# Kernel tuning notes

Measured on AMD Instinct MI355X. Metric: run time of the kernel, lower is better.

## Reference

```python
import jax, jax.numpy as jnp
import numpy as np

POOL = (32, 32, 32)
P_ENC_DIM = 48
NON_LOCAL_ITER = 2


def _neighbor_graph(spatial):
    # connectivity=2 binary structure in 3x3x3 (k_size=3): 19 offsets with |dx|+|dy|+|dz| <= 2
    D, H, W = spatial
    offs = np.array([(dx, dy, dz) for dx in (-1, 0, 1) for dy in (-1, 0, 1) for dz in (-1, 0, 1)
                     if abs(dx) + abs(dy) + abs(dz) <= 2], dtype=np.int64)  # [K=19,3]
    coords = np.stack(np.meshgrid(np.arange(D), np.arange(H), np.arange(W), indexing='ij'), -1).reshape(-1, 3)
    nbr = coords[:, None, :] + offs[None]                                  # [N,K,3]
    valid = ((nbr >= 0) & (nbr < np.array([D, H, W]))).all(-1)             # [N,K] side nodes lose oob edges
    nbrc = np.clip(nbr, 0, np.array([D - 1, H - 1, W - 1]))
    idx = np.ravel_multi_index(nbrc.reshape(-1, 3).T, (D, H, W)).reshape(valid.shape)
    return jnp.asarray(idx, jnp.int32), jnp.asarray(valid)


def _build_pe(spatial, p_enc_dim, dtype=jnp.float32):
    # sin/cos positional encoding over 3D grid, interleaved per axis (build_geo_feature)
    D, H, W = spatial
    d_model = p_enc_dim // 3
    div = (1e-4) ** (jnp.arange(0, d_model, 2, dtype=dtype) / d_model)     # [d_model//2]
    grids = jnp.meshgrid(jnp.arange(D), jnp.arange(H), jnp.arange(W), indexing='ij')
    parts = []
    for d in range(3):
        ang = grids[d].astype(dtype)[None] * div[:, None, None, None]      # [h,D,H,W]
        parts.append(jnp.stack([jnp.sin(ang), jnp.cos(ang)], 1).reshape(d_model, D, H, W))
    pe = jnp.concatenate(parts, 0)                                         # [p_enc_dim,D,H,W]
    return pe.reshape(p_enc_dim, -1).T                                     # [N,p_enc_dim]


def setup_inputs():
    key = jax.random.key(0)
    ks = jax.random.split(key, 6)
    B, Cf, Cc, FD, GD = 2, 256, 21, 64, 64
    D, H, W = POOL
    neighbor_idx, nbr_mask = _neighbor_graph(POOL)

    def lin(k, fi, fo):
        return jax.random.normal(k, (fi, fo), jnp.float32) / np.sqrt(fi).astype(np.float32)

    return {
        'cam': jax.random.uniform(ks[0], (B, Cc, D, H, W), jnp.float32),
        'f': jax.random.normal(ks[1], (B, Cf, D, H, W), jnp.float32),
        'theta_w': lin(ks[2], Cf, FD), 'theta_b': jnp.zeros((FD,), jnp.float32),
        'phi_w': lin(ks[3], Cf, FD), 'phi_b': jnp.zeros((FD,), jnp.float32),
        'geo_theta_w': lin(ks[4], P_ENC_DIM, GD), 'geo_theta_b': jnp.zeros((GD,), jnp.float32),
        'geo_phi_w': lin(ks[5], P_ENC_DIM, GD), 'geo_phi_b': jnp.zeros((GD,), jnp.float32),
        'neighbor_idx': neighbor_idx, 'nbr_mask': nbr_mask,
    }


def reference(cam, f, theta_w, theta_b, phi_w, phi_b, geo_theta_w, geo_theta_b,
              geo_phi_w, geo_phi_b, neighbor_idx, nbr_mask):
    B, Cc, D, H, W = cam.shape
    N = D * H * W
    f_flat = f.reshape(B, f.shape[1], N).transpose(0, 2, 1)                # [B,N,Cf]
    x_theta = f_flat @ theta_w + theta_b                                    # [B,N,fd]
    x_phi = (f_flat @ phi_w + phi_b)[:, neighbor_idx]                       # [B,N,K,fd] gather
    pe = jax.lax.stop_gradient(_build_pe((D, H, W), P_ENC_DIM, cam.dtype))  # geo feature is detached
    g_theta = pe @ geo_theta_w + geo_theta_b                                # [N,gd]
    g_phi = (pe @ geo_phi_w + geo_phi_b)[neighbor_idx]                      # [N,K,gd]
    # merge_type 'scaled_dot_product_geo': f = theta.phi + geo_theta.geo_phi; softmax(f / sqrt(K))
    scores = jnp.einsum('bnd,bnkd->bnk', x_theta, x_phi) \
           + jnp.einsum('nd,nkd->nk', g_theta, g_phi)[None]
    Kn = scores.shape[-1]
    scores = scores / jnp.sqrt(jnp.asarray(Kn, scores.dtype))
    scores = jnp.where(nbr_mask[None], scores, -jnp.inf)                    # side nodes: fewer edges
    w = jax.nn.softmax(scores, axis=-1)                                     # [B,N,K]
    cam_flat = cam.reshape(B, Cc, N).transpose(0, 2, 1)                     # [B,N,Cc]
    for _ in range(NON_LOCAL_ITER):                                         # weights fixed (f unchanged)
        cam_flat = jnp.einsum('bnk,bnkc->bnc', w, cam_flat[:, neighbor_idx])
    return cam_flat.transpose(0, 2, 1).reshape(B, Cc, D, H, W)
```

## Files before the change

kernel.cpp:

```cpp
#include <hip/hip_runtime.h>
#include <hip/hip_bf16.h>
#include <hip/hip_fp16.h>

#define DD 32
#define HH 32
#define WW 32
#define NN 32768
#define BB 2
#define CF 256
#define CC 21
#define FD 64
#define KK 19

typedef __attribute__((ext_vector_type(8))) short bf16x8;
typedef __attribute__((ext_vector_type(4))) float f32x4;

__device__ const int OFF[19][3] = {
    {-1,-1, 0}, {-1, 0,-1}, {-1, 0, 0}, {-1, 0, 1}, {-1, 1, 0},
    { 0,-1,-1}, { 0,-1, 0}, { 0,-1, 1}, { 0, 0,-1}, { 0, 0, 0},
    { 0, 0, 1}, { 0, 1,-1}, { 0, 1, 0}, { 0, 1, 1},
    { 1,-1, 0}, { 1, 0,-1}, { 1, 0, 0}, { 1, 0, 1}, { 1, 1, 0}
};

__device__ __forceinline__ unsigned short f2bf(float x) {
    unsigned u = __float_as_uint(x);
    u += 0x7FFFu + ((u >> 16) & 1u);
    return (unsigned short)(u >> 16);
}

__global__ __launch_bounds__(256) void tbl_kernel(
    const float* __restrict__ gtw, const float* __restrict__ gtb,
    const float* __restrict__ gpw, const float* __restrict__ gpb,
    const float* __restrict__ thw, const float* __restrict__ phw,
    float* __restrict__ Tg, uint4* __restrict__ whi)
{
    int blk = blockIdx.x, tid = threadIdx.x;
    if (blk >= 10) {
        int gid = (blk - 10) * 256 + tid;
        int col = gid & 127;
        int g8 = gid >> 7;
        const float* src = (col < 64) ? (thw + col) : (phw + (col - 64));
        int kbase = g8 * 8;
        unsigned hi4[4];
#pragma unroll
        for (int e2 = 0; e2 < 4; ++e2) {
            float va = src[(kbase + 2 * e2) * 64];
            float vb = src[(kbase + 2 * e2 + 1) * 64];
            hi4[e2] = (unsigned)f2bf(va) | ((unsigned)f2bf(vb) << 16);
        }
        whi[g8 * 128 + col] = make_uint4(hi4[0], hi4[1], hi4[2], hi4[3]);
        return;
    }

    __shared__ float pe_s[32][16];
    for (int i = tid; i < 512; i += 256) {
        int c = i >> 4, q = i & 15;
        int ii = q >> 1;
        float div = expf(-9.210340371976184f * (float)ii * 0.125f);
        float ang = (float)c * div;
        pe_s[c][q] = (q & 1) ? cosf(ang) : sinf(ang);
    }
    __syncthreads();

    __shared__ float panels[6][32][65];
    int npan = (blk == 9) ? 6 : 2;
#pragma unroll 1
    for (int pp = 0; pp < npan; ++pp) {
        int axis, isP;
        if (blk == 9) { axis = pp % 3; isP = pp / 3; }
        else          { axis = (pp == 0) ? (blk / 3) : (blk % 3); isP = pp; }
        const float* W = isP ? gpw : gtw;
#pragma unroll
        for (int e = 0; e < 8; ++e) {
            int idx = e * 256 + tid;
            int c = idx >> 6, j = idx & 63;
            float acc = 0.f;
#pragma unroll
            for (int q = 0; q < 16; ++q)
                acc = fmaf(pe_s[c][q], W[(axis * 16 + q) * 64 + j], acc);
            panels[pp][c][j] = acc;
        }
    }
    __syncthreads();

    if (blk < 9) {
        bool tr = (blk == 6) || (blk == 7);
#pragma unroll
        for (int e = 0; e < 4; ++e) {
            int idx = e * 256 + tid;
            int x = idx >> 5, y = idx & 31;
            float s = 0.f;
#pragma unroll
            for (int j = 0; j < 64; ++j)
                s = fmaf(panels[0][x][j], panels[1][y][j], s);
            Tg[blk * 1024 + (tr ? (y * 32 + x) : (x * 32 + y))] = s;
        }
    } else {
        if (tid < 96) {
            int ax = tid >> 5, c = tid & 31;
            float s = 0.f;
#pragma unroll
            for (int j = 0; j < 64; ++j) s = fmaf(panels[ax][c][j], gpb[j], s);
            Tg[9216 + ax * 32 + c] = s;
        } else if (tid < 192) {
            int t2 = tid - 96;
            int ax = t2 >> 5, c = t2 & 31;
            float s = 0.f;
#pragma unroll
            for (int j = 0; j < 64; ++j) s = fmaf(gtb[j], panels[3 + ax][c][j], s);
            Tg[9312 + ax * 32 + c] = s;
        } else if (tid == 192) {
            float s = 0.f;
#pragma unroll
            for (int j = 0; j < 64; ++j) s = fmaf(gtb[j], gpb[j], s);
            Tg[9408] = s;
        }
    }
}

__global__ __launch_bounds__(256) void proj_kernel(
    const float* __restrict__ f, const uint4* __restrict__ whi,
    const float* __restrict__ thb, const float* __restrict__ phb,
    __half* __restrict__ theta, __half* __restrict__ phi)
{
    __shared__ __align__(16) unsigned short Ahi[128][8][8];
    __shared__ __align__(16) unsigned short Bhi[128][8][8];

    int tid = threadIdx.x;
    int b = blockIdx.x >> 8;
    int n0 = (blockIdx.x & 255) * 128;
    int wv = tid >> 6, lane = tid & 63;
    int wr = (wv >> 1) * 64, wc = (wv & 1) * 64;
    int fr = lane & 15, kb_r = lane >> 4;

    int srow = tid & 127;
    int kb0 = (tid >> 7) * 4;

    const float* fb = f + (size_t)b * CF * NN + n0;

    f32x4 acc[4][4];
#pragma unroll
    for (int mi = 0; mi < 4; ++mi)
#pragma unroll
        for (int ni = 0; ni < 4; ++ni) acc[mi][ni] = (f32x4){0.f, 0.f, 0.f, 0.f};

#pragma unroll 1
    for (int k0 = 0; k0 < CF; k0 += 64) {
#pragma unroll
        for (int i = 0; i < 4; ++i) {
            int kb = kb0 + i;
            const float* src = fb + (size_t)(k0 + kb * 8) * NN + srow;
            unsigned hi4[4];
#pragma unroll
            for (int e2 = 0; e2 < 4; ++e2) {
                float va = src[(size_t)(2 * e2) * NN];
                float vb = src[(size_t)(2 * e2 + 1) * NN];
                hi4[e2] = (unsigned)f2bf(va) | ((unsigned)f2bf(vb) << 16);
            }
            int slot = kb ^ (srow & 7);
            *(uint4*)&Ahi[srow][slot][0] = make_uint4(hi4[0], hi4[1], hi4[2], hi4[3]);
        }
        {
            const uint4* wh = whi + (size_t)(k0 >> 3) * 128;
#pragma unroll
            for (int i = 0; i < 4; ++i) {
                int kb = kb0 + i;
                uint4 hh = wh[kb * 128 + srow];
                int slot = kb ^ (srow & 7);
                *(uint4*)&Bhi[srow][slot][0] = hh;
            }
        }
        __syncthreads();
#pragma unroll
        for (int c = 0; c < 2; ++c) {
            bf16x8 ah[4], bh[4];
            int kb_c = c * 4 + kb_r;
#pragma unroll
            for (int mi = 0; mi < 4; ++mi) {
                int r = wr + mi * 16 + fr;
                int slot = kb_c ^ (r & 7);
                ah[mi] = *(const bf16x8*)&Ahi[r][slot][0];
            }
#pragma unroll
            for (int ni = 0; ni < 4; ++ni) {
                int col = wc + ni * 16 + fr;
                int slot = kb_c ^ (col & 7);
                bh[ni] = *(const bf16x8*)&Bhi[col][slot][0];
            }
#pragma unroll
            for (int mi = 0; mi < 4; ++mi)
#pragma unroll
                for (int ni = 0; ni < 4; ++ni)
                    acc[mi][ni] = __builtin_amdgcn_mfma_f32_16x16x32_bf16(ah[mi], bh[ni], acc[mi][ni], 0, 0, 0);
        }
        __syncthreads();
    }

#pragma unroll
    for (int ni = 0; ni < 4; ++ni) {
        int j = wc + ni * 16 + fr;
        float bj = (j < 64) ? thb[j] : phb[j - 64];
        __half* outp = (j < 64) ? (theta + (size_t)b * NN * 64 + j)
                                : (phi + (size_t)b * NN * 64 + (j - 64));
#pragma unroll
        for (int mi = 0; mi < 4; ++mi) {
            int nbase = n0 + wr + mi * 16 + kb_r * 4;
#pragma unroll
            for (int r = 0; r < 4; ++r)
                outp[(size_t)(nbase + r) * 64] = __float2half(acc[mi][ni][r] + bj);
        }
    }
}

__global__ __launch_bounds__(256) void gsc_kernel(
    const float* __restrict__ Tg, float* __restrict__ gsc)
{
    __shared__ float Ts[9 * 1024];
    __shared__ float UVs[193];
    int tid = threadIdx.x;
#pragma unroll
    for (int i = 0; i < 9; ++i) {
        int idx = i * 1024 + tid;
        Ts[idx] = Tg[idx];
        Ts[idx + 256] = Tg[idx + 256];
        Ts[idx + 512] = Tg[idx + 512];
        Ts[idx + 768] = Tg[idx + 768];
    }
    if (tid < 193) UVs[tid] = Tg[9216 + tid];
    __syncthreads();

    int n = blockIdx.x * 256 + tid;
    int d = n >> 10, h = (n >> 5) & 31, w = n & 31;
    float Un = UVs[d] + UVs[32 + h] + UVs[64 + w] + UVs[192];
    const float rs = 0.2294157338705618f;

#pragma unroll
    for (int k = 0; k < KK; ++k) {
        int nd = d + OFF[k][0], nh = h + OFF[k][1], nw = w + OFF[k][2];
        bool valid = ((unsigned)nd < 32u) && ((unsigned)nh < 32u) && ((unsigned)nw < 32u);
        int ndc = min(max(nd, 0), 31), nhc = min(max(nh, 0), 31), nwc = min(max(nw, 0), 31);
        float g = Ts[0 * 1024 + d * 32 + ndc] + Ts[1 * 1024 + d * 32 + nhc]
                + Ts[2 * 1024 + d * 32 + nwc] + Ts[3 * 1024 + h * 32 + ndc]
                + Ts[4 * 1024 + h * 32 + nhc] + Ts[5 * 1024 + h * 32 + nwc]
                + Ts[6 * 1024 + ndc * 32 + w] + Ts[7 * 1024 + nhc * 32 + w]
                + Ts[8 * 1024 + w * 32 + nwc]
                + Un + UVs[96 + ndc] + UVs[128 + nhc] + UVs[160 + nwc];
        gsc[(size_t)k * NN + n] = valid ? g * rs : -INFINITY;
    }
}

__global__ __launch_bounds__(256) void score_kernel(
    const __half* __restrict__ theta, const __half* __restrict__ phi,
    const float* __restrict__ gsc, float* __restrict__ wgt)
{
    int tid = threadIdx.x;
    int lane = tid & 63;
    int wv = tid >> 6;
    int sub = lane >> 4;
    int col4 = lane & 15;
    int gn = blockIdx.x * 16 + wv * 4 + sub;
    int b = gn >> 15;
    int n = gn & (NN - 1);
    int d = n >> 10, h = (n >> 5) & 31, w = n & 31;

    uint2 traw = *(const uint2*)(theta + (size_t)gn * 64 + col4 * 4);
    __half2 t01 = __builtin_bit_cast(__half2, traw.x);
    __half2 t23 = __builtin_bit_cast(__half2, traw.y);
    float2 tf01 = __half22float2(t01), tf23 = __half22float2(t23);
    float4 tq = {tf01.x, tf01.y, tf23.x, tf23.y};

    const __half* pb = phi + (size_t)b * NN * 64;
    const float* gr = gsc + n;
    const float rs = 0.2294157338705618f;

    float s[KK];
#pragma unroll
    for (int k = 0; k < KK; ++k) {
        int nd = d + OFF[k][0], nh = h + OFF[k][1], nw = w + OFF[k][2];
        nd = min(max(nd, 0), 31); nh = min(max(nh, 0), 31); nw = min(max(nw, 0), 31);
        int nn = (nd << 10) + (nh << 5) + nw;
        uint2 raw = *(const uint2*)(pb + (size_t)nn * 64 + col4 * 4);
        __half2 h01 = __builtin_bit_cast(__half2, raw.x);
        __half2 h23 = __builtin_bit_cast(__half2, raw.y);
        float2 f01 = __half22float2(h01), f23 = __half22float2(h23);
        float part = tq.x * f01.x + tq.y * f01.y + tq.z * f23.x + tq.w * f23.y;
        part += __shfl_xor(part, 1, 16);
        part += __shfl_xor(part, 2, 16);
        part += __shfl_xor(part, 4, 16);
        part += __shfl_xor(part, 8, 16);
        s[k] = fmaf(part, rs, gr[(size_t)k * NN]);
    }
    float m = s[0];
#pragma unroll
    for (int k = 1; k < KK; ++k) m = fmaxf(m, s[k]);
    float sum = 0.f;
#pragma unroll
    for (int k = 0; k < KK; ++k) { s[k] = __expf(s[k] - m); sum += s[k]; }
    float inv = 1.f / sum;
#pragma unroll
    for (int kk2 = 0; kk2 < 2; ++kk2) {
        int k = kk2 * 16 + col4;
        if (k < KK) wgt[((size_t)b * KK + k) * NN + n] = s[k] * inv;
    }
}

__global__ __launch_bounds__(256) void prop_kernel(
    const float* __restrict__ cin, const float* __restrict__ wgt,
    float* __restrict__ cout)
{
    int gid = blockIdx.x * 256 + threadIdx.x;
    int n = gid & (NN - 1);
    int rest = gid >> 15;
    int b = rest / 3, cg = rest % 3;
    int c0 = cg * 7;
    int d = n >> 10, h = (n >> 5) & 31, w = n & 31;

    const float* wb = wgt + (size_t)b * KK * NN + n;
    int nidx[KK];
    float wv[KK];
#pragma unroll
    for (int k = 0; k < KK; ++k) {
        int nd = d + OFF[k][0], nh = h + OFF[k][1], nw = w + OFF[k][2];
        nd = min(max(nd, 0), 31); nh = min(max(nh, 0), 31); nw = min(max(nw, 0), 31);
        nidx[k] = (nd << 10) + (nh << 5) + nw;
        wv[k] = wb[(size_t)k * NN];
    }

    const float* cb = cin + ((size_t)b * CC + c0) * NN;
    float* co = cout + ((size_t)b * CC + c0) * NN + n;
#pragma unroll
    for (int cc = 0; cc < 7; ++cc) {
        float acc = 0.f;
#pragma unroll
        for (int k = 0; k < KK; ++k)
            acc = fmaf(wv[k], cb[nidx[k]], acc);
        co[(size_t)cc * NN] = acc;
        cb += NN;
    }
}

extern "C" void kernel_launch(void* const* d_in, const int* in_sizes, int n_in,
                              void* d_out, int out_size, void* d_ws, size_t ws_size,
                              hipStream_t stream) {
    const float* cam = (const float*)d_in[0];
    const float* f   = (const float*)d_in[1];
    const float* thw = (const float*)d_in[2];
    const float* thb = (const float*)d_in[3];
    const float* phw = (const float*)d_in[4];
    const float* phb = (const float*)d_in[5];
    const float* gtw = (const float*)d_in[6];
    const float* gtb = (const float*)d_in[7];
    const float* gpw = (const float*)d_in[8];
    const float* gpb = (const float*)d_in[9];

    float*  ws    = (float*)d_ws;
    __half* theta = (__half*)ws;
    __half* phi   = theta + (size_t)BB * NN * 64;
    float*  wgt   = (float*)(phi + (size_t)BB * NN * 64);
    float*  gsc   = wgt + (size_t)BB * KK * NN;
    float*  cam1  = gsc + (size_t)KK * NN;
    uint4*  whi   = (uint4*)(cam1 + (size_t)BB * CC * NN);
    float*  Tg    = (float*)(whi + 4096);

    tbl_kernel<<<26, 256, 0, stream>>>(gtw, gtb, gpw, gpb, thw, phw, Tg, whi);
    proj_kernel<<<512, 256, 0, stream>>>(f, whi, thb, phb, theta, phi);
    gsc_kernel<<<NN / 256, 256, 0, stream>>>(Tg, gsc);
    score_kernel<<<BB * NN / 16, 256, 0, stream>>>(theta, phi, gsc, wgt);
    prop_kernel<<<BB * NN * 3 / 256, 256, 0, stream>>>(cam, wgt, cam1);
    prop_kernel<<<BB * NN * 3 / 256, 256, 0, stream>>>(cam1, wgt, (float*)d_out);
}
```

Baseline: 67.23 us.

## Fuse both propagation iterations into one halo-tiled kernel; halve projection tile

The two propagation passes are merged into one kernel. Each block loads its 4x8x8 tile plus halo of weights and cam into LDS, computes the intermediate on a 6x10x10 halo region, then produces the final output, so the cam1 intermediate never touches global memory. The projection GEMM tile is also cut from 128 to 64 rows, doubling the block count to improve occupancy. The fused kernel launches only 256 blocks and loops serially over 21 channels with two barriers each, and it recomputes the halo, which may limit parallelism.

```diff
diff --git a/kernel.cpp b/kernel.cpp
--- a/kernel.cpp
+++ b/kernel.cpp
@@ -123,33 +123,35 @@
     const float* __restrict__ thb, const float* __restrict__ phb,
     __half* __restrict__ theta, __half* __restrict__ phi)
 {
-    __shared__ __align__(16) unsigned short Ahi[128][8][8];
+    __shared__ __align__(16) unsigned short Ahi[64][8][8];
     __shared__ __align__(16) unsigned short Bhi[128][8][8];
 
     int tid = threadIdx.x;
-    int b = blockIdx.x >> 8;
-    int n0 = (blockIdx.x & 255) * 128;
+    int b = blockIdx.x >> 9;
+    int n0 = (blockIdx.x & 511) * 64;
     int wv = tid >> 6, lane = tid & 63;
-    int wr = (wv >> 1) * 64, wc = (wv & 1) * 64;
+    int wr = (wv & 1) * 32, wc = (wv >> 1) * 64;
     int fr = lane & 15, kb_r = lane >> 4;
 
-    int srow = tid & 127;
-    int kb0 = (tid >> 7) * 4;
+    int arow = tid & 63;
+    int akb0 = (tid >> 6) * 2;
+    int bcol = tid & 127;
+    int bkb0 = (tid >> 7) * 4;
 
     const float* fb = f + (size_t)b * CF * NN + n0;
 
-    f32x4 acc[4][4];
-#pragma unroll
-    for (int mi = 0; mi < 4; ++mi)
+    f32x4 acc[2][4];
+#pragma unroll
+    for (int mi = 0; mi < 2; ++mi)
 #pragma unroll
         for (int ni = 0; ni < 4; ++ni) acc[mi][ni] = (f32x4){0.f, 0.f, 0.f, 0.f};
 
 #pragma unroll 1
     for (int k0 = 0; k0 < CF; k0 += 64) {
 #pragma unroll
-        for (int i = 0; i < 4; ++i) {
-            int kb = kb0 + i;
-            const float* src = fb + (size_t)(k0 + kb * 8) * NN + srow;
+        for (int i = 0; i < 2; ++i) {
+            int kb = akb0 + i;
+            const float* src = fb + (size_t)(k0 + kb * 8) * NN + arow;
             unsigned hi4[4];
 #pragma unroll
             for (int e2 = 0; e2 < 4; ++e2) {
@@ -157,26 +159,26 @@
                 float vb = src[(size_t)(2 * e2 + 1) * NN];
                 hi4[e2] = (unsigned)f2bf(va) | ((unsigned)f2bf(vb) << 16);
             }
-            int slot = kb ^ (srow & 7);
-            *(uint4*)&Ahi[srow][slot][0] = make_uint4(hi4[0], hi4[1], hi4[2], hi4[3]);
+            int slot = kb ^ (arow & 7);
+            *(uint4*)&Ahi[arow][slot][0] = make_uint4(hi4[0], hi4[1], hi4[2], hi4[3]);
         }
         {
             const uint4* wh = whi + (size_t)(k0 >> 3) * 128;
 #pragma unroll
             for (int i = 0; i < 4; ++i) {
-                int kb = kb0 + i;
-                uint4 hh = wh[kb * 128 + srow];
-                int slot = kb ^ (srow & 7);
-                *(uint4*)&Bhi[srow][slot][0] = hh;
+                int kb = bkb0 + i;
+                uint4 hh = wh[kb * 128 + bcol];
+                int slot = kb ^ (bcol & 7);
+                *(uint4*)&Bhi[bcol][slot][0] = hh;
             }
         }
         __syncthreads();
 #pragma unroll
         for (int c = 0; c < 2; ++c) {
-            bf16x8 ah[4], bh[4];
+            bf16x8 ah[2], bh[4];
             int kb_c = c * 4 + kb_r;
 #pragma unroll
-            for (int mi = 0; mi < 4; ++mi) {
+            for (int mi = 0; mi < 2; ++mi) {
                 int r = wr + mi * 16 + fr;
                 int slot = kb_c ^ (r & 7);
                 ah[mi] = *(const bf16x8*)&Ahi[r][slot][0];
@@ -188,7 +190,7 @@
                 bh[ni] = *(const bf16x8*)&Bhi[col][slot][0];
             }
 #pragma unroll
-            for (int mi = 0; mi < 4; ++mi)
+            for (int mi = 0; mi < 2; ++mi)
 #pragma unroll
                 for (int ni = 0; ni < 4; ++ni)
                     acc[mi][ni] = __builtin_amdgcn_mfma_f32_16x16x32_bf16(ah[mi], bh[ni], acc[mi][ni], 0, 0, 0);
@@ -203,7 +205,7 @@
         __half* outp = (j < 64) ? (theta + (size_t)b * NN * 64 + j)
                                 : (phi + (size_t)b * NN * 64 + (j - 64));
 #pragma unroll
-        for (int mi = 0; mi < 4; ++mi) {
+        for (int mi = 0; mi < 2; ++mi) {
             int nbase = n0 + wr + mi * 16 + kb_r * 4;
 #pragma unroll
             for (int r = 0; r < 4; ++r)
@@ -304,38 +306,62 @@
     }
 }
 
-__global__ __launch_bounds__(256) void prop_kernel(
-    const float* __restrict__ cin, const float* __restrict__ wgt,
+__global__ __launch_bounds__(256) void prop2_kernel(
+    const float* __restrict__ cam, const float* __restrict__ wgt,
     float* __restrict__ cout)
 {
-    int gid = blockIdx.x * 256 + threadIdx.x;
-    int n = gid & (NN - 1);
-    int rest = gid >> 15;
-    int b = rest / 3, cg = rest % 3;
-    int c0 = cg * 7;
-    int d = n >> 10, h = (n >> 5) & 31, w = n & 31;
-
-    const float* wb = wgt + (size_t)b * KK * NN + n;
-    int nidx[KK];
-    float wv[KK];
-#pragma unroll
-    for (int k = 0; k < KK; ++k) {
-        int nd = d + OFF[k][0], nh = h + OFF[k][1], nw = w + OFF[k][2];
-        nd = min(max(nd, 0), 31); nh = min(max(nh, 0), 31); nw = min(max(nw, 0), 31);
-        nidx[k] = (nd << 10) + (nh << 5) + nw;
-        wv[k] = wb[(size_t)k * NN];
-    }
-
-    const float* cb = cin + ((size_t)b * CC + c0) * NN;
-    float* co = cout + ((size_t)b * CC + c0) * NN + n;
-#pragma unroll
-    for (int cc = 0; cc < 7; ++cc) {
-        float acc = 0.f;
-#pragma unroll
-        for (int k = 0; k < KK; ++k)
-            acc = fmaf(wv[k], cb[nidx[k]], acc);
-        co[(size_t)cc * NN] = acc;
-        cb += NN;
+    __shared__ float Wlds[KK][600];
+    __shared__ float camt[8 * 12 * 12];
+    __shared__ float inter[6 * 10 * 10];
+    int blk = blockIdx.x;
+    int tile = blk & 127;
+    int b = blk >> 7;
+    int tw = tile & 3, th = (tile >> 2) & 3, td = tile >> 4;
+    int d0 = td * 4, h0 = th * 8, w0 = tw * 8;
+    int tid = threadIdx.x;
+
+    const float* wb = wgt + (size_t)b * KK * NN;
+    for (int i = tid; i < 600 * KK; i += 256) {
+        int k = i / 600, j = i - k * 600;
+        int lw = j % 10, lh = (j / 10) % 10, ld = j / 100;
+        int gd = min(max(d0 - 1 + ld, 0), 31);
+        int gh = min(max(h0 - 1 + lh, 0), 31);
+        int gw = min(max(w0 - 1 + lw, 0), 31);
+        Wlds[k][j] = wb[(size_t)k * NN + (gd << 10) + (gh << 5) + gw];
+    }
+
+    int flw = tid & 7, flh = (tid >> 3) & 7, fld = tid >> 6;
+    int fj = (fld + 1) * 100 + (flh + 1) * 10 + (flw + 1);
+    int fn = ((d0 + fld) << 10) + ((h0 + flh) << 5) + (w0 + flw);
+
+#pragma unroll 1
+    for (int c = 0; c < CC; ++c) {
+        const float* cb = cam + ((size_t)b * CC + c) * NN;
+        for (int i = tid; i < 1152; i += 256) {
+            int lw = i % 12, lh = (i / 12) % 12, ld = i / 144;
+            int gd = min(max(d0 - 2 + ld, 0), 31);
+            int gh = min(max(h0 - 2 + lh, 0), 31);
+            int gw = min(max(w0 - 2 + lw, 0), 31);
+            camt[i] = cb[(gd << 10) + (gh << 5) + gw];
+        }
+        __syncthreads();
+        for (int i = tid; i < 600; i += 256) {
+            int lw = i % 10, lh = (i / 10) % 10, ld = i / 100;
+            int cbase = (ld + 1) * 144 + (lh + 1) * 12 + (lw + 1);
+            float acc = 0.f;
+#pragma unroll
+            for (int k = 0; k < KK; ++k)
+                acc = fmaf(Wlds[k][i], camt[cbase + OFF[k][0] * 144 + OFF[k][1] * 12 + OFF[k][2]], acc);
+            inter[i] = acc;
+        }
+        __syncthreads();
+        {
+            float acc = 0.f;
+#pragma unroll
+            for (int k = 0; k < KK; ++k)
+                acc = fmaf(Wlds[k][fj], inter[fj + OFF[k][0] * 100 + OFF[k][1] * 10 + OFF[k][2]], acc);
+            cout[((size_t)b * CC + c) * NN + fn] = acc;
+        }
     }
 }
 
@@ -358,14 +384,12 @@
     __half* phi   = theta + (size_t)BB * NN * 64;
     float*  wgt   = (float*)(phi + (size_t)BB * NN * 64);
     float*  gsc   = wgt + (size_t)BB * KK * NN;
-    float*  cam1  = gsc + (size_t)KK * NN;
-    uint4*  whi   = (uint4*)(cam1 + (size_t)BB * CC * NN);
+    uint4*  whi   = (uint4*)(gsc + (size_t)KK * NN);
     float*  Tg    = (float*)(whi + 4096);
 
     tbl_kernel<<<26, 256, 0, stream>>>(gtw, gtb, gpw, gpb, thw, phw, Tg, whi);
-    proj_kernel<<<512, 256, 0, stream>>>(f, whi, thb, phb, theta, phi);
+    proj_kernel<<<1024, 256, 0, stream>>>(f, whi, thb, phb, theta, phi);
     gsc_kernel<<<NN / 256, 256, 0, stream>>>(Tg, gsc);
     score_kernel<<<BB * NN / 16, 256, 0, stream>>>(theta, phi, gsc, wgt);
-    prop_kernel<<<BB * NN * 3 / 256, 256, 0, stream>>>(cam, wgt, cam1);
-    prop_kernel<<<BB * NN * 3 / 256, 256, 0, stream>>>(cam1, wgt, (float*)d_out);
-}
+    prop2_kernel<<<BB * 128, 256, 0, stream>>>(cam, wgt, (float*)d_out);
+}
```

Result: slower. 128.5 us (+91.1%).
